# Kernel tuning notes

Measured on AMD Instinct MI355X. Metric: run time of the kernel, lower is better.

## Reference

```python
import math
import jax, jax.numpy as jnp
import numpy as np

D_MODEL = 1024
NUM_HEADS = 16
HEAD_DIM = D_MODEL // NUM_HEADS
CAUSAL = True


def setup_inputs() -> dict:
    key = jax.random.key(0)
    ks = jax.random.split(key, 9)
    B, S = 2, 2048
    s = 1.0 / math.sqrt(D_MODEL)
    x = jax.random.normal(ks[0], (B, S, D_MODEL), dtype=jnp.float32)
    Wq = jax.random.normal(ks[1], (D_MODEL, D_MODEL), dtype=jnp.float32) * s
    bq = jax.random.normal(ks[2], (D_MODEL,), dtype=jnp.float32) * 0.01
    Wk = jax.random.normal(ks[3], (D_MODEL, D_MODEL), dtype=jnp.float32) * s
    bk = jax.random.normal(ks[4], (D_MODEL,), dtype=jnp.float32) * 0.01
    Wv = jax.random.normal(ks[5], (D_MODEL, D_MODEL), dtype=jnp.float32) * s
    bv = jax.random.normal(ks[6], (D_MODEL,), dtype=jnp.float32) * 0.01
    Wo = jax.random.normal(ks[7], (D_MODEL, D_MODEL), dtype=jnp.float32) * s
    bo = jax.random.normal(ks[8], (D_MODEL,), dtype=jnp.float32) * 0.01
    return {"x": x, "Wq": Wq, "bq": bq, "Wk": Wk, "bk": bk,
            "Wv": Wv, "bv": bv, "Wo": Wo, "bo": bo}


def reference(x, Wq, bq, Wk, bk, Wv, bv, Wo, bo):
    B, S, _ = x.shape
    # projections (torch Linear: x @ W.T + b; here W already stored as [in,out])
    q = x @ Wq + bq
    k = x @ Wk + bk
    v = x @ Wv + bv
    # split heads -> [B, H, S, hd]
    def split(t):
        return t.reshape(B, S, NUM_HEADS, HEAD_DIM).transpose(0, 2, 1, 3)
    q, k, v = split(q), split(k), split(v)
    scores = jnp.einsum('bhqd,bhkd->bhqk', q, k) / math.sqrt(HEAD_DIM)
    if CAUSAL:
        causal = jnp.tril(jnp.ones((S, S), dtype=bool))  # True = keep
        scores = jnp.where(causal, scores, -jnp.inf)
    attn = jax.nn.softmax(scores, axis=-1)
    out = jnp.einsum('bhqk,bhkd->bhqd', attn, v)
    out = out.transpose(0, 2, 1, 3).reshape(B, S, D_MODEL)
    return out @ Wo + bo
```

## Files before the change

### kernel.cpp

```cpp
#include <hip/hip_runtime.h>
#include <hip/hip_bf16.h>

typedef __bf16 bf16_t;
typedef __bf16 v8bf __attribute__((ext_vector_type(8)));
typedef float  v4f  __attribute__((ext_vector_type(4)));

#define MFMA16(a, b, c) __builtin_amdgcn_mfma_f32_16x16x32_bf16((a), (b), (c), 0, 0, 0)

#define GLDS16(g, l) __builtin_amdgcn_global_load_lds(                         \
    (const __attribute__((address_space(1))) void*)(g),                        \
    (__attribute__((address_space(3))) void*)(l), 16, 0, 0)

#define VMEMCNT(n) asm volatile("s_waitcnt vmcnt(" #n ")" ::: "memory")
#define SBAR()     __builtin_amdgcn_s_barrier()
#define SFENCE()   __builtin_amdgcn_sched_barrier(0)

#define B_SZ   2
#define SEQ    2048
#define DM     1024
#define NH     16
#define HD     64
#define M_TOT  4096

#define QSCALE 0.18033688011112043f

__global__ __launch_bounds__(256)
void conv_x_kernel(const float* __restrict__ src, bf16_t* __restrict__ dst)
{
    int i = (blockIdx.x * 256 + threadIdx.x) * 8;
    float4 a = *reinterpret_cast<const float4*>(src + i);
    float4 b = *reinterpret_cast<const float4*>(src + i + 4);
    union { bf16_t h[8]; int4 v; } u;
    u.h[0] = (bf16_t)a.x; u.h[1] = (bf16_t)a.y; u.h[2] = (bf16_t)a.z; u.h[3] = (bf16_t)a.w;
    u.h[4] = (bf16_t)b.x; u.h[5] = (bf16_t)b.y; u.h[6] = (bf16_t)b.z; u.h[7] = (bf16_t)b.w;
    *reinterpret_cast<int4*>(dst + i) = u.v;
}

__global__ __launch_bounds__(256)
void conv_wt_kernel(const float* __restrict__ Wq, const float* __restrict__ Wk,
                    const float* __restrict__ Wv, const float* __restrict__ Wo,
                    bf16_t* __restrict__ WqkvT, bf16_t* __restrict__ WoT)
{
    __shared__ float t[32][33];
    const int z = blockIdx.z;
    const float* src = (z == 0) ? Wq : (z == 1) ? Wk : (z == 2) ? Wv : Wo;
    bf16_t* dst = (z < 3) ? (WqkvT + (size_t)z * 1048576) : WoT;
    const int tx = threadIdx.x & 31, ty = threadIdx.x >> 5;
    const int c0 = blockIdx.x * 32, r0 = blockIdx.y * 32;
#pragma unroll
    for (int i = 0; i < 4; ++i)
        t[ty + i * 8][tx] = src[(size_t)(r0 + ty + i * 8) * DM + c0 + tx];
    __syncthreads();
#pragma unroll
    for (int i = 0; i < 4; ++i)
        dst[(size_t)(c0 + ty + i * 8) * DM + r0 + tx] = (bf16_t)t[tx][ty + i * 8];
}

__global__ __launch_bounds__(256)
void gemm_qkv_kernel(const bf16_t* __restrict__ A, const bf16_t* __restrict__ BT,
                     const float* __restrict__ b0, const float* __restrict__ b1,
                     const float* __restrict__ b2,
                     bf16_t* __restrict__ oQ, bf16_t* __restrict__ oK,
                     bf16_t* __restrict__ oV)
{
    __shared__ __align__(16) bf16_t As[2 * 128 * 64];
    __shared__ __align__(16) bf16_t Bs[2 * 192 * 64];

    const int tid  = threadIdx.x;
    const int lane = tid & 63;
    const int wave = tid >> 6;
    const int wm   = (wave >> 1) * 64;
    const int wn   = (wave & 1) * 96;
    const int quad = lane >> 4;
    const int l15  = lane & 15;
    const int l7   = l15 & 7;

    const int n0 = blockIdx.x * 192;
    const int m0 = blockIdx.y * 128;

    const bf16_t *ap[4], *bp[6];
#pragma unroll
    for (int i = 0; i < 4; ++i) {
        int cidx = (wave * 4 + i) * 64 + lane;
        int r = cidx >> 3;
        int c = (cidx & 7) ^ (r & 7);
        ap[i] = A + (size_t)(m0 + r) * DM + c * 8;
    }
#pragma unroll
    for (int i = 0; i < 6; ++i) {
        int cidx = (wave * 6 + i) * 64 + lane;
        int r = cidx >> 3;
        int c = (cidx & 7) ^ (r & 7);
        bp[i] = BT + (size_t)(n0 + r) * DM + c * 8;
    }

    const v4f vzero = {0.f, 0.f, 0.f, 0.f};
    v4f acc[4][6];
#pragma unroll
    for (int mt = 0; mt < 4; ++mt)
#pragma unroll
        for (int nt = 0; nt < 6; ++nt) acc[mt][nt] = vzero;

#pragma unroll
    for (int i = 0; i < 4; ++i) { GLDS16(ap[i], As + (wave * 4 + i) * 512); ap[i] += 64; }
#pragma unroll
    for (int i = 0; i < 6; ++i) { GLDS16(bp[i], Bs + (wave * 6 + i) * 512); bp[i] += 64; }
#pragma unroll
    for (int i = 0; i < 4; ++i) { GLDS16(ap[i], As + 8192 + (wave * 4 + i) * 512); ap[i] += 64; }
#pragma unroll
    for (int i = 0; i < 6; ++i) { GLDS16(bp[i], Bs + 12288 + (wave * 6 + i) * 512); bp[i] += 64; }

    for (int it = 0; it < 16; ++it) {
        const int cur = it & 1;
        if (it < 15) { VMEMCNT(10); } else { VMEMCNT(0); }
        SBAR(); SFENCE();
#pragma unroll
        for (int ks = 0; ks < 2; ++ks) {
            v8bf af[4], bfq[6];
#pragma unroll
            for (int mt = 0; mt < 4; ++mt)
                af[mt] = *reinterpret_cast<const v8bf*>(
                    &As[cur * 8192 + (wm + mt * 16 + l15) * 64 + ((ks * 4 + quad) ^ l7) * 8]);
#pragma unroll
            for (int nt = 0; nt < 6; ++nt)
                bfq[nt] = *reinterpret_cast<const v8bf*>(
                    &Bs[cur * 12288 + (wn + nt * 16 + l15) * 64 + ((ks * 4 + quad) ^ l7) * 8]);
#pragma unroll
            for (int mt = 0; mt < 4; ++mt)
#pragma unroll
                for (int nt = 0; nt < 6; ++nt)
                    acc[mt][nt] = MFMA16(bfq[nt], af[mt], acc[mt][nt]);
        }
        SFENCE(); SBAR();
        if (it < 14) {
#pragma unroll
            for (int i = 0; i < 4; ++i) {
                GLDS16(ap[i], As + cur * 8192 + (wave * 4 + i) * 512);
                ap[i] += 64;
            }
#pragma unroll
            for (int i = 0; i < 6; ++i) {
                GLDS16(bp[i], Bs + cur * 12288 + (wave * 6 + i) * 512);
                bp[i] += 64;
            }
        }
    }

#pragma unroll
    for (int nt = 0; nt < 6; ++nt) {
        const int cf0 = n0 + wn + nt * 16;
        const int mat = cf0 >> 10;
        const int cw  = cf0 & 1023;
        if (mat != 2) {
            bf16_t* dst = (mat == 0) ? oQ : oK;
            const float scale = (mat == 0) ? QSCALE : 1.0f;
            const float* bias = (mat == 0) ? b0 : b1;
            const int h = cw >> 6;
            const int dbase = (cw & 63) + quad * 4;
            float4 bv = *reinterpret_cast<const float4*>(bias + cw + quad * 4);
#pragma unroll
            for (int mt = 0; mt < 4; ++mt) {
                int srow = m0 + wm + mt * 16 + l15;
                int b = srow >> 11, s = srow & 2047;
                union { bf16_t hh[4]; int2 v; } u;
                u.hh[0] = (bf16_t)((acc[mt][nt][0] + bv.x) * scale);
                u.hh[1] = (bf16_t)((acc[mt][nt][1] + bv.y) * scale);
                u.hh[2] = (bf16_t)((acc[mt][nt][2] + bv.z) * scale);
                u.hh[3] = (bf16_t)((acc[mt][nt][3] + bv.w) * scale);
                *reinterpret_cast<int2*>(
                    dst + ((size_t)(b * NH + h) * SEQ + s) * HD + dbase) = u.v;
            }
        } else {
#pragma unroll
            for (int r = 0; r < 4; ++r) {
                int cwe = cw + quad * 4 + r;
                float bvv = b2[cwe];
                int h = cwe >> 6, d = cwe & 63;
#pragma unroll
                for (int mt = 0; mt < 4; ++mt) {
                    int srow = m0 + wm + mt * 16 + l15;
                    int b = srow >> 11, s = srow & 2047;
                    oV[((size_t)(b * NH + h) * HD + d) * SEQ + s] =
                        (bf16_t)(acc[mt][nt][r] + bvv);
                }
            }
        }
    }
}

__global__ __launch_bounds__(256)
void gemm_o_kernel(const bf16_t* __restrict__ A, const bf16_t* __restrict__ BT,
                   const float* __restrict__ bias, float* __restrict__ out)
{
    __shared__ __align__(16) bf16_t As[2 * 128 * 64];
    __shared__ __align__(16) bf16_t Bs[2 * 64 * 64];

    const int tid  = threadIdx.x;
    const int lane = tid & 63;
    const int wave = tid >> 6;
    const int wm   = (wave >> 1) * 64;
    const int wn   = (wave & 1) * 32;
    const int quad = lane >> 4;
    const int l15  = lane & 15;
    const int l7   = l15 & 7;

    const int n0 = blockIdx.x * 64;
    const int m0 = blockIdx.y * 128;

    const bf16_t *ap[4], *bp[2];
#pragma unroll
    for (int i = 0; i < 4; ++i) {
        int cidx = (wave * 4 + i) * 64 + lane;
        int r = cidx >> 3;
        int c = (cidx & 7) ^ (r & 7);
        ap[i] = A + (size_t)(m0 + r) * DM + c * 8;
    }
#pragma unroll
    for (int i = 0; i < 2; ++i) {
        int cidx = (wave * 2 + i) * 64 + lane;
        int r = cidx >> 3;
        int c = (cidx & 7) ^ (r & 7);
        bp[i] = BT + (size_t)(n0 + r) * DM + c * 8;
    }

    const v4f vzero = {0.f, 0.f, 0.f, 0.f};
    v4f acc[4][2];
#pragma unroll
    for (int mt = 0; mt < 4; ++mt)
#pragma unroll
        for (int nt = 0; nt < 2; ++nt) acc[mt][nt] = vzero;

#pragma unroll
    for (int i = 0; i < 4; ++i) { GLDS16(ap[i], As + (wave * 4 + i) * 512); ap[i] += 64; }
#pragma unroll
    for (int i = 0; i < 2; ++i) { GLDS16(bp[i], Bs + (wave * 2 + i) * 512); bp[i] += 64; }
#pragma unroll
    for (int i = 0; i < 4; ++i) { GLDS16(ap[i], As + 8192 + (wave * 4 + i) * 512); ap[i] += 64; }
#pragma unroll
    for (int i = 0; i < 2; ++i) { GLDS16(bp[i], Bs + 4096 + (wave * 2 + i) * 512); bp[i] += 64; }

    for (int it = 0; it < 16; ++it) {
        const int cur = it & 1;
        if (it < 15) { VMEMCNT(6); } else { VMEMCNT(0); }
        SBAR(); SFENCE();
#pragma unroll
        for (int ks = 0; ks < 2; ++ks) {
            v8bf af[4], bfq[2];
#pragma unroll
            for (int mt = 0; mt < 4; ++mt)
                af[mt] = *reinterpret_cast<const v8bf*>(
                    &As[cur * 8192 + (wm + mt * 16 + l15) * 64 + ((ks * 4 + quad) ^ l7) * 8]);
#pragma unroll
            for (int nt = 0; nt < 2; ++nt)
                bfq[nt] = *reinterpret_cast<const v8bf*>(
                    &Bs[cur * 4096 + (wn + nt * 16 + l15) * 64 + ((ks * 4 + quad) ^ l7) * 8]);
#pragma unroll
            for (int mt = 0; mt < 4; ++mt)
#pragma unroll
                for (int nt = 0; nt < 2; ++nt)
                    acc[mt][nt] = MFMA16(af[mt], bfq[nt], acc[mt][nt]);
        }
        SFENCE(); SBAR();
        if (it < 14) {
#pragma unroll
            for (int i = 0; i < 4; ++i) {
                GLDS16(ap[i], As + cur * 8192 + (wave * 4 + i) * 512);
                ap[i] += 64;
            }
#pragma unroll
            for (int i = 0; i < 2; ++i) {
                GLDS16(bp[i], Bs + cur * 4096 + (wave * 2 + i) * 512);
                bp[i] += 64;
            }
        }
    }

#pragma unroll
    for (int mt = 0; mt < 4; ++mt) {
#pragma unroll
        for (int nt = 0; nt < 2; ++nt) {
            int col = n0 + wn + nt * 16 + l15;
            float bv = bias[col];
#pragma unroll
            for (int r = 0; r < 4; ++r) {
                int row = m0 + wm + mt * 16 + quad * 4 + r;
                out[(size_t)row * DM + col] = acc[mt][nt][r] + bv;
            }
        }
    }
}

__global__ __launch_bounds__(256)
void attn_kernel(const bf16_t* __restrict__ Q, const bf16_t* __restrict__ K,
                 const bf16_t* __restrict__ Vt, bf16_t* __restrict__ O)
{
    __shared__ __align__(16) bf16_t Ks[4][64 * 64];
    __shared__ __align__(16) bf16_t Vs[4][64 * 64];
    float* Ored = reinterpret_cast<float*>(&Ks[0][0]);
    float* lred = reinterpret_cast<float*>(&Vs[0][0]);

    const int tid  = threadIdx.x;
    const int lane = tid & 63;
    const int w    = tid >> 6;
    const int quad = lane >> 4;
    const int l15  = lane & 15;
    const int l7   = lane & 7;

    const int bid = blockIdx.x;
    const int xcd = bid & 7;
    const int j   = bid >> 3;
    const int bh  = (xcd << 2) | (j >> 4);
    const int p   = j & 15;
    const size_t base = (size_t)bh * SEQ * HD;
    const bf16_t* Qg = Q  + base;
    const bf16_t* Kg = K  + base;
    const bf16_t* Vg = Vt + base;

    const int rr0 = tid >> 3;
    const int cc0 = (tid & 7) ^ (rr0 & 7);
    const int bO = bh >> 4, hO = bh & 15;
    const v4f vzero = {0.f, 0.f, 0.f, 0.f};

    for (int phase = 0; phase < 2; ++phase) {
        const int t  = phase ? (31 - p) : p;
        const int q0 = t * 64;
        const int ns = (t + 2) >> 1;
        const bool tEven = ((t & 1) == 0);

        v8bf qf[4][2];
#pragma unroll
        for (int g = 0; g < 4; ++g) {
            const bf16_t* qrow = Qg + (size_t)(q0 + g * 16 + l15) * HD;
            qf[g][0] = *reinterpret_cast<const v8bf*>(qrow + quad * 8);
            qf[g][1] = *reinterpret_cast<const v8bf*>(qrow + 32 + quad * 8);
        }

        const bf16_t* kp0 = Kg + (size_t)rr0 * HD + cc0 * 8;
        const bf16_t* kp1 = kp0 + 32 * HD;
        const bf16_t* vp0 = Vg + (size_t)rr0 * SEQ + cc0 * 8;
        const bf16_t* vp1 = vp0 + (size_t)32 * SEQ;

        v4f acc_p[4][4];
#pragma unroll
        for (int dt = 0; dt < 4; ++dt)
#pragma unroll
            for (int g = 0; g < 4; ++g) acc_p[dt][g] = vzero;
        float lp[4] = {0.f, 0.f, 0.f, 0.f};

        VMEMCNT(0);
        SBAR();

#pragma unroll
        for (int s = 0; s < 2; ++s) {
            GLDS16(kp0, &Ks[s][w * 512]);  GLDS16(kp1, &Ks[s][2048 + w * 512]);
            GLDS16(vp0, &Vs[s][w * 512]);  GLDS16(vp1, &Vs[s][2048 + w * 512]);
            kp0 += 64 * HD;  kp1 += 64 * HD;  vp0 += 64;  vp1 += 64;
        }
        if (ns > 1) {
#pragma unroll
            for (int s = 2; s < 4; ++s) {
                GLDS16(kp0, &Ks[s][w * 512]);  GLDS16(kp1, &Ks[s][2048 + w * 512]);
                GLDS16(vp0, &Vs[s][w * 512]);  GLDS16(vp1, &Vs[s][2048 + w * 512]);
                kp0 += 64 * HD;  kp1 += 64 * HD;  vp0 += 64;  vp1 += 64;
            }
        }

        for (int si = 0; si < ns; ++si) {
            const int sA = (si & 1) * 2, sB = sA + 1;
            if (si + 1 < ns) { VMEMCNT(8); } else { VMEMCNT(0); }
            SBAR(); SFENCE();

            const bool last  = (si == ns - 1);
            const bool diagA = last && tEven;
            const bool diagB = last && !tEven;

            v4f stA[4], stB[4];
#pragma unroll
            for (int g = 0; g < 4; ++g) { stA[g] = vzero; stB[g] = vzero; }
#pragma unroll
            for (int ks = 0; ks < 2; ++ks) {
                const int koff = (16 * w + l15) * 64 + ((ks * 4 + quad) ^ l7) * 8;
                v8bf kfA = *reinterpret_cast<const v8bf*>(&Ks[sA][koff]);
                v8bf kfB = *reinterpret_cast<const v8bf*>(&Ks[sB][koff]);
#pragma unroll
                for (int g = 0; g < 4; ++g) {
                    stA[g] = MFMA16(kfA, qf[g][ks], stA[g]);
                    stB[g] = MFMA16(kfB, qf[g][ks], stB[g]);
                }
            }

            v8bf pa[4];
#pragma unroll
            for (int g = 0; g < 4; ++g) {
                union { bf16_t h[8]; v8bf v; } up;
                if (diagA && g < w) {
                    up.h[0] = (bf16_t)0.f; up.h[1] = (bf16_t)0.f;
                    up.h[2] = (bf16_t)0.f; up.h[3] = (bf16_t)0.f;
                } else if (diagA && g == w) {
#pragma unroll
                    for (int r = 0; r < 4; ++r) {
                        float pv = (quad * 4 + r > l15)
                                     ? 0.f : __builtin_amdgcn_exp2f(stA[g][r]);
                        lp[g] += pv;
                        up.h[r] = (bf16_t)pv;
                    }
                } else {
#pragma unroll
                    for (int r = 0; r < 4; ++r) {
                        float pv = __builtin_amdgcn_exp2f(stA[g][r]);
                        lp[g] += pv;
                        up.h[r] = (bf16_t)pv;
                    }
                }
                if (diagA || (diagB && g < w)) {
                    up.h[4] = (bf16_t)0.f; up.h[5] = (bf16_t)0.f;
                    up.h[6] = (bf16_t)0.f; up.h[7] = (bf16_t)0.f;
                } else if (diagB && g == w) {
#pragma unroll
                    for (int r = 0; r < 4; ++r) {
                        float pv = (quad * 4 + r > l15)
                                     ? 0.f : __builtin_amdgcn_exp2f(stB[g][r]);
                        lp[g] += pv;
                        up.h[4 + r] = (bf16_t)pv;
                    }
                } else {
#pragma unroll
                    for (int r = 0; r < 4; ++r) {
                        float pv = __builtin_amdgcn_exp2f(stB[g][r]);
                        lp[g] += pv;
                        up.h[4 + r] = (bf16_t)pv;
                    }
                }
                pa[g] = up.v;
            }

#pragma unroll
            for (int dt = 0; dt < 4; ++dt) {
                const int rowd = dt * 16 + l15;
                const int voff = rowd * 64 +
                    (((2 * w + (quad >> 1)) ^ l7) * 8 + (quad & 1) * 4);
                uint2 va = *reinterpret_cast<const uint2*>(&Vs[sA][voff]);
                uint2 vb = *reinterpret_cast<const uint2*>(&Vs[sB][voff]);
                union { unsigned u[4]; v8bf v; } uv;
                uv.u[0] = va.x; uv.u[1] = va.y; uv.u[2] = vb.x; uv.u[3] = vb.y;
#pragma unroll
                for (int g = 0; g < 4; ++g)
                    acc_p[dt][g] = MFMA16(uv.v, pa[g], acc_p[dt][g]);
            }

            SFENCE(); SBAR();
            if (si + 2 < ns) {
                GLDS16(kp0, &Ks[sA][w * 512]);  GLDS16(kp1, &Ks[sA][2048 + w * 512]);
                GLDS16(vp0, &Vs[sA][w * 512]);  GLDS16(vp1, &Vs[sA][2048 + w * 512]);
                kp0 += 64 * HD;  kp1 += 64 * HD;  vp0 += 64;  vp1 += 64;
                GLDS16(kp0, &Ks[sB][w * 512]);  GLDS16(kp1, &Ks[sB][2048 + w * 512]);
                GLDS16(vp0, &Vs[sB][w * 512]);  GLDS16(vp1, &Vs[sB][2048 + w * 512]);
                kp0 += 64 * HD;  kp1 += 64 * HD;  vp0 += 64;  vp1 += 64;
            }
        }

#pragma unroll
        for (int g = 0; g < 4; ++g) {
            lp[g] += __shfl_xor(lp[g], 16);
            lp[g] += __shfl_xor(lp[g], 32);
        }
        if (quad == 0) {
#pragma unroll
            for (int g = 0; g < 4; ++g)
                lred[w * 64 + g * 16 + l15] = lp[g];
        }

        const int qq = tid >> 2;
        const int db = (tid & 3) * 4;
        float linv = 0.f;
#pragma unroll
        for (int dt = 0; dt < 4; ++dt) {
#pragma unroll
            for (int g = 0; g < 4; ++g)
#pragma unroll
                for (int r = 0; r < 4; ++r)
                    Ored[w * 1040 + (quad * 4 + r) * 65 + g * 16 + l15] =
                        acc_p[dt][g][r];
            SBAR();
            if (dt == 0)
                linv = 1.f / (lred[qq] + lred[64 + qq] +
                              lred[128 + qq] + lred[192 + qq]);
            union { bf16_t h[4]; int2 v; } u;
#pragma unroll
            for (int e = 0; e < 4; ++e) {
                float s = Ored[(db + e) * 65 + qq]
                        + Ored[1040 + (db + e) * 65 + qq]
                        + Ored[2080 + (db + e) * 65 + qq]
                        + Ored[3120 + (db + e) * 65 + qq];
                u.h[e] = (bf16_t)(s * linv);
            }
            *reinterpret_cast<int2*>(
                &O[((size_t)bO * SEQ + q0 + qq) * DM + hO * 64 + dt * 16 + db]) = u.v;
            SBAR();
        }
    }
}

extern "C" void kernel_launch(void* const* d_in, const int* in_sizes, int n_in,
                              void* d_out, int out_size, void* d_ws, size_t ws_size,
                              hipStream_t stream) {
    const float* x  = (const float*)d_in[0];
    const float* Wq = (const float*)d_in[1];
    const float* bq = (const float*)d_in[2];
    const float* Wk = (const float*)d_in[3];
    const float* bk = (const float*)d_in[4];
    const float* Wv = (const float*)d_in[5];
    const float* bv = (const float*)d_in[6];
    const float* Wo = (const float*)d_in[7];
    const float* bo = (const float*)d_in[8];

    bf16_t* ws = (bf16_t*)d_ws;
    bf16_t* xb     = ws;
    bf16_t* WqkvT  = ws + 4194304;
    bf16_t* WoT    = ws + 7340032;
    bf16_t* Qb     = ws + 8388608;
    bf16_t* Kb     = ws + 12582912;
    bf16_t* Vb     = ws + 16777216;
    bf16_t* Ob     = ws;

    conv_x_kernel<<<2048, 256, 0, stream>>>(x, xb);
    conv_wt_kernel<<<dim3(32, 32, 4), 256, 0, stream>>>(Wq, Wk, Wv, Wo, WqkvT, WoT);
    gemm_qkv_kernel<<<dim3(16, 32), 256, 0, stream>>>(xb, WqkvT, bq, bk, bv, Qb, Kb, Vb);
    attn_kernel<<<512, 256, 0, stream>>>(Qb, Kb, Vb, Ob);
    gemm_o_kernel<<<dim3(16, 32), 256, 0, stream>>>(Ob, WoT, bo, (float*)d_out);
}
```

Baseline: 173.8 us.

## Shrink GEMM tiles and drop LDS double buffering to raise block count

The QKV GEMM moves from 128x192 tiles to 128x128 tiles, with one Q, K or V matrix per block column, giving a 24x32 grid. The O-projection GEMM moves to 64x64 tiles with 128 threads, giving a 16x64 grid. Both kernels drop the double-buffered LDS pipeline and its explicit vmcnt waits for a single buffer guarded by __syncthreads. The aim is more blocks and occupancy on the many-CU device, at the cost of exposed load latency and less operand reuse per tile.

```diff
diff --git a/kernel.cpp b/kernel.cpp
--- a/kernel.cpp
+++ b/kernel.cpp
@@ -63,101 +63,86 @@
                      bf16_t* __restrict__ oQ, bf16_t* __restrict__ oK,
                      bf16_t* __restrict__ oV)
 {
-    __shared__ __align__(16) bf16_t As[2 * 128 * 64];
-    __shared__ __align__(16) bf16_t Bs[2 * 192 * 64];
+    __shared__ __align__(16) bf16_t As[128 * 64];
+    __shared__ __align__(16) bf16_t Bs[128 * 64];
 
     const int tid  = threadIdx.x;
     const int lane = tid & 63;
     const int wave = tid >> 6;
     const int wm   = (wave >> 1) * 64;
-    const int wn   = (wave & 1) * 96;
+    const int wn   = (wave & 1) * 64;
     const int quad = lane >> 4;
     const int l15  = lane & 15;
     const int l7   = l15 & 7;
 
-    const int n0 = blockIdx.x * 192;
-    const int m0 = blockIdx.y * 128;
-
-    const bf16_t *ap[4], *bp[6];
+    const int mat = blockIdx.x >> 3;
+    const int n0  = (blockIdx.x & 7) * 128;
+    const int m0  = blockIdx.y * 128;
+    const bf16_t* Bmat = BT + (size_t)mat * 1048576;
+
+    const bf16_t *ap[4], *bp[4];
 #pragma unroll
     for (int i = 0; i < 4; ++i) {
         int cidx = (wave * 4 + i) * 64 + lane;
         int r = cidx >> 3;
         int c = (cidx & 7) ^ (r & 7);
-        ap[i] = A + (size_t)(m0 + r) * DM + c * 8;
-    }
-#pragma unroll
-    for (int i = 0; i < 6; ++i) {
-        int cidx = (wave * 6 + i) * 64 + lane;
-        int r = cidx >> 3;
-        int c = (cidx & 7) ^ (r & 7);
-        bp[i] = BT + (size_t)(n0 + r) * DM + c * 8;
+        ap[i] = A    + (size_t)(m0 + r) * DM + c * 8;
+        bp[i] = Bmat + (size_t)(n0 + r) * DM + c * 8;
     }
 
     const v4f vzero = {0.f, 0.f, 0.f, 0.f};
-    v4f acc[4][6];
+    v4f acc[4][4];
 #pragma unroll
     for (int mt = 0; mt < 4; ++mt)
 #pragma unroll
-        for (int nt = 0; nt < 6; ++nt) acc[mt][nt] = vzero;
-
-#pragma unroll
-    for (int i = 0; i < 4; ++i) { GLDS16(ap[i], As + (wave * 4 + i) * 512); ap[i] += 64; }
-#pragma unroll
-    for (int i = 0; i < 6; ++i) { GLDS16(bp[i], Bs + (wave * 6 + i) * 512); bp[i] += 64; }
-#pragma unroll
-    for (int i = 0; i < 4; ++i) { GLDS16(ap[i], As + 8192 + (wave * 4 + i) * 512); ap[i] += 64; }
-#pragma unroll
-    for (int i = 0; i < 6; ++i) { GLDS16(bp[i], Bs + 12288 + (wave * 6 + i) * 512); bp[i] += 64; }
+        for (int nt = 0; nt < 4; ++nt) acc[mt][nt] = vzero;
+
+#pragma unroll
+    for (int i = 0; i < 4; ++i) {
+        GLDS16(ap[i], As + (wave * 4 + i) * 512);
+        GLDS16(bp[i], Bs + (wave * 4 + i) * 512);
+        ap[i] += 64; bp[i] += 64;
+    }
 
     for (int it = 0; it < 16; ++it) {
-        const int cur = it & 1;
-        if (it < 15) { VMEMCNT(10); } else { VMEMCNT(0); }
-        SBAR(); SFENCE();
+        __syncthreads();
 #pragma unroll
         for (int ks = 0; ks < 2; ++ks) {
-            v8bf af[4], bfq[6];
+            v8bf af[4], bfq[4];
 #pragma unroll
             for (int mt = 0; mt < 4; ++mt)
                 af[mt] = *reinterpret_cast<const v8bf*>(
-                    &As[cur * 8192 + (wm + mt * 16 + l15) * 64 + ((ks * 4 + quad) ^ l7) * 8]);
-#pragma unroll
-            for (int nt = 0; nt < 6; ++nt)
+                    &As[(wm + mt * 16 + l15) * 64 + ((ks * 4 + quad) ^ l7) * 8]);
+#pragma unroll
+            for (int nt = 0; nt < 4; ++nt)
                 bfq[nt] = *reinterpret_cast<const v8bf*>(
-                    &Bs[cur * 12288 + (wn + nt * 16 + l15) * 64 + ((ks * 4 + quad) ^ l7) * 8]);
+                    &Bs[(wn + nt * 16 + l15) * 64 + ((ks * 4 + quad) ^ l7) * 8]);
 #pragma unroll
             for (int mt = 0; mt < 4; ++mt)
 #pragma unroll
-                for (int nt = 0; nt < 6; ++nt)
+                for (int nt = 0; nt < 4; ++nt)
                     acc[mt][nt] = MFMA16(bfq[nt], af[mt], acc[mt][nt]);
         }
-        SFENCE(); SBAR();
-        if (it < 14) {
+        __syncthreads();
+        if (it < 15) {
 #pragma unroll
             for (int i = 0; i < 4; ++i) {
-                GLDS16(ap[i], As + cur * 8192 + (wave * 4 + i) * 512);
-                ap[i] += 64;
-            }
-#pragma unroll
-            for (int i = 0; i < 6; ++i) {
-                GLDS16(bp[i], Bs + cur * 12288 + (wave * 6 + i) * 512);
-                bp[i] += 64;
-            }
-        }
-    }
-
-#pragma unroll
-    for (int nt = 0; nt < 6; ++nt) {
-        const int cf0 = n0 + wn + nt * 16;
-        const int mat = cf0 >> 10;
-        const int cw  = cf0 & 1023;
-        if (mat != 2) {
-            bf16_t* dst = (mat == 0) ? oQ : oK;
-            const float scale = (mat == 0) ? QSCALE : 1.0f;
-            const float* bias = (mat == 0) ? b0 : b1;
-            const int h = cw >> 6;
-            const int dbase = (cw & 63) + quad * 4;
-            float4 bv = *reinterpret_cast<const float4*>(bias + cw + quad * 4);
+                GLDS16(ap[i], As + (wave * 4 + i) * 512);
+                GLDS16(bp[i], Bs + (wave * 4 + i) * 512);
+                ap[i] += 64; bp[i] += 64;
+            }
+        }
+    }
+
+    const float* bias = (mat == 0) ? b0 : (mat == 1) ? b1 : b2;
+    if (mat != 2) {
+        bf16_t* dst = (mat == 0) ? oQ : oK;
+        const float scale = (mat == 0) ? QSCALE : 1.0f;
+        const int h = (n0 + wn) >> 6;
+#pragma unroll
+        for (int nt = 0; nt < 4; ++nt) {
+            const int dbase = nt * 16 + quad * 4;
+            float4 bv = *reinterpret_cast<const float4*>(bias + n0 + wn + dbase);
 #pragma unroll
             for (int mt = 0; mt < 4; ++mt) {
                 int srow = m0 + wm + mt * 16 + l15;
@@ -170,116 +155,104 @@
                 *reinterpret_cast<int2*>(
                     dst + ((size_t)(b * NH + h) * SEQ + s) * HD + dbase) = u.v;
             }
-        } else {
+        }
+    } else {
+#pragma unroll
+        for (int nt = 0; nt < 4; ++nt) {
 #pragma unroll
             for (int r = 0; r < 4; ++r) {
-                int cwe = cw + quad * 4 + r;
-                float bvv = b2[cwe];
-                int h = cwe >> 6, d = cwe & 63;
+                int coln = n0 + wn + nt * 16 + quad * 4 + r;
+                float bv = bias[coln];
+                int h = coln >> 6, d = coln & 63;
 #pragma unroll
                 for (int mt = 0; mt < 4; ++mt) {
                     int srow = m0 + wm + mt * 16 + l15;
                     int b = srow >> 11, s = srow & 2047;
                     oV[((size_t)(b * NH + h) * HD + d) * SEQ + s] =
-                        (bf16_t)(acc[mt][nt][r] + bvv);
+                        (bf16_t)(acc[mt][nt][r] + bv);
                 }
             }
         }
     }
 }
 
-__global__ __launch_bounds__(256)
+__global__ __launch_bounds__(128)
 void gemm_o_kernel(const bf16_t* __restrict__ A, const bf16_t* __restrict__ BT,
                    const float* __restrict__ bias, float* __restrict__ out)
 {
-    __shared__ __align__(16) bf16_t As[2 * 128 * 64];
-    __shared__ __align__(16) bf16_t Bs[2 * 64 * 64];
+    __shared__ __align__(16) bf16_t As[64 * 64];
+    __shared__ __align__(16) bf16_t Bs[64 * 64];
 
     const int tid  = threadIdx.x;
     const int lane = tid & 63;
     const int wave = tid >> 6;
-    const int wm   = (wave >> 1) * 64;
-    const int wn   = (wave & 1) * 32;
+    const int wm   = wave * 32;
     const int quad = lane >> 4;
     const int l15  = lane & 15;
     const int l7   = l15 & 7;
 
     const int n0 = blockIdx.x * 64;
-    const int m0 = blockIdx.y * 128;
-
-    const bf16_t *ap[4], *bp[2];
+    const int m0 = blockIdx.y * 64;
+
+    const bf16_t *ap[4], *bp[4];
 #pragma unroll
     for (int i = 0; i < 4; ++i) {
-        int cidx = (wave * 4 + i) * 64 + lane;
+        int cidx = wave * 64 + i * 128 + lane;
         int r = cidx >> 3;
         int c = (cidx & 7) ^ (r & 7);
-        ap[i] = A + (size_t)(m0 + r) * DM + c * 8;
-    }
-#pragma unroll
-    for (int i = 0; i < 2; ++i) {
-        int cidx = (wave * 2 + i) * 64 + lane;
-        int r = cidx >> 3;
-        int c = (cidx & 7) ^ (r & 7);
+        ap[i] = A  + (size_t)(m0 + r) * DM + c * 8;
         bp[i] = BT + (size_t)(n0 + r) * DM + c * 8;
     }
 
     const v4f vzero = {0.f, 0.f, 0.f, 0.f};
-    v4f acc[4][2];
-#pragma unroll
-    for (int mt = 0; mt < 4; ++mt)
-#pragma unroll
-        for (int nt = 0; nt < 2; ++nt) acc[mt][nt] = vzero;
-
-#pragma unroll
-    for (int i = 0; i < 4; ++i) { GLDS16(ap[i], As + (wave * 4 + i) * 512); ap[i] += 64; }
-#pragma unroll
-    for (int i = 0; i < 2; ++i) { GLDS16(bp[i], Bs + (wave * 2 + i) * 512); bp[i] += 64; }
-#pragma unroll
-    for (int i = 0; i < 4; ++i) { GLDS16(ap[i], As + 8192 + (wave * 4 + i) * 512); ap[i] += 64; }
-#pragma unroll
-    for (int i = 0; i < 2; ++i) { GLDS16(bp[i], Bs + 4096 + (wave * 2 + i) * 512); bp[i] += 64; }
+    v4f acc[2][4];
+#pragma unroll
+    for (int mt = 0; mt < 2; ++mt)
+#pragma unroll
+        for (int nt = 0; nt < 4; ++nt) acc[mt][nt] = vzero;
+
+#pragma unroll
+    for (int i = 0; i < 4; ++i) {
+        GLDS16(ap[i], As + wave * 512 + i * 1024);
+        GLDS16(bp[i], Bs + wave * 512 + i * 1024);
+        ap[i] += 64; bp[i] += 64;
+    }
 
     for (int it = 0; it < 16; ++it) {
-        const int cur = it & 1;
-        if (it < 15) { VMEMCNT(6); } else { VMEMCNT(0); }
-        SBAR(); SFENCE();
+        __syncthreads();
 #pragma unroll
         for (int ks = 0; ks < 2; ++ks) {
-            v8bf af[4], bfq[2];
-#pragma unroll
-            for (int mt = 0; mt < 4; ++mt)
+            v8bf af[2], bfq[4];
+#pragma unroll
+            for (int mt = 0; mt < 2; ++mt)
                 af[mt] = *reinterpret_cast<const v8bf*>(
-                    &As[cur * 8192 + (wm + mt * 16 + l15) * 64 + ((ks * 4 + quad) ^ l7) * 8]);
-#pragma unroll
-            for (int nt = 0; nt < 2; ++nt)
+                    &As[(wm + mt * 16 + l15) * 64 + ((ks * 4 + quad) ^ l7) * 8]);
+#pragma unroll
+            for (int nt = 0; nt < 4; ++nt)
                 bfq[nt] = *reinterpret_cast<const v8bf*>(
-                    &Bs[cur * 4096 + (wn + nt * 16 + l15) * 64 + ((ks * 4 + quad) ^ l7) * 8]);
-#pragma unroll
-            for (int mt = 0; mt < 4; ++mt)
-#pragma unroll
-                for (int nt = 0; nt < 2; ++nt)
+                    &Bs[(nt * 16 + l15) * 64 + ((ks * 4 + quad) ^ l7) * 8]);
+#pragma unroll
+            for (int mt = 0; mt < 2; ++mt)
+#pragma unroll
+                for (int nt = 0; nt < 4; ++nt)
                     acc[mt][nt] = MFMA16(af[mt], bfq[nt], acc[mt][nt]);
         }
-        SFENCE(); SBAR();
-        if (it < 14) {
+        __syncthreads();
+        if (it < 15) {
 #pragma unroll
             for (int i = 0; i < 4; ++i) {
-                GLDS16(ap[i], As + cur * 8192 + (wave * 4 + i) * 512);
-                ap[i] += 64;
-            }
-#pragma unroll
-            for (int i = 0; i < 2; ++i) {
-                GLDS16(bp[i], Bs + cur * 4096 + (wave * 2 + i) * 512);
-                bp[i] += 64;
-            }
-        }
-    }
-
-#pragma unroll
-    for (int mt = 0; mt < 4; ++mt) {
-#pragma unroll
-        for (int nt = 0; nt < 2; ++nt) {
-            int col = n0 + wn + nt * 16 + l15;
+                GLDS16(ap[i], As + wave * 512 + i * 1024);
+                GLDS16(bp[i], Bs + wave * 512 + i * 1024);
+                ap[i] += 64; bp[i] += 64;
+            }
+        }
+    }
+
+#pragma unroll
+    for (int mt = 0; mt < 2; ++mt) {
+#pragma unroll
+        for (int nt = 0; nt < 4; ++nt) {
+            int col = n0 + nt * 16 + l15;
             float bv = bias[col];
 #pragma unroll
             for (int r = 0; r < 4; ++r) {
@@ -525,7 +498,7 @@
 
     conv_x_kernel<<<2048, 256, 0, stream>>>(x, xb);
     conv_wt_kernel<<<dim3(32, 32, 4), 256, 0, stream>>>(Wq, Wk, Wv, Wo, WqkvT, WoT);
-    gemm_qkv_kernel<<<dim3(16, 32), 256, 0, stream>>>(xb, WqkvT, bq, bk, bv, Qb, Kb, Vb);
+    gemm_qkv_kernel<<<dim3(24, 32), 256, 0, stream>>>(xb, WqkvT, bq, bk, bv, Qb, Kb, Vb);
     attn_kernel<<<512, 256, 0, stream>>>(Qb, Kb, Vb, Ob);
-    gemm_o_kernel<<<dim3(16, 32), 256, 0, stream>>>(Ob, WoT, bo, (float*)d_out);
+    gemm_o_kernel<<<dim3(16, 64), 128, 0, stream>>>(Ob, WoT, bo, (float*)d_out);
 }
```

Measured after the change: 180.3 us. 3.7% more time.

## Shrink output-projection GEMM tile to 64x64 with two waves and single buffer

Applied to the files above, without the earlier changes.

The output-projection GEMM tile shrinks from 128x64 to 64x64 and runs on 128 threads (two waves, each computing 32x64), which doubles the grid to 1024 blocks. The LDS double buffer and its explicit vmcnt waits are replaced by one buffer guarded by __syncthreads. The goal is better fill across the GPU's compute units, with less LDS and register use per block. In exchange, loads no longer overlap compute within a block, each tile reuses less data, and more global traffic goes to re-reading A and B.

```diff
diff --git a/kernel.cpp b/kernel.cpp
--- a/kernel.cpp
+++ b/kernel.cpp
@@ -188,98 +188,83 @@
     }
 }
 
-__global__ __launch_bounds__(256)
+__global__ __launch_bounds__(128)
 void gemm_o_kernel(const bf16_t* __restrict__ A, const bf16_t* __restrict__ BT,
                    const float* __restrict__ bias, float* __restrict__ out)
 {
-    __shared__ __align__(16) bf16_t As[2 * 128 * 64];
-    __shared__ __align__(16) bf16_t Bs[2 * 64 * 64];
+    __shared__ __align__(16) bf16_t As[64 * 64];
+    __shared__ __align__(16) bf16_t Bs[64 * 64];
 
     const int tid  = threadIdx.x;
     const int lane = tid & 63;
     const int wave = tid >> 6;
-    const int wm   = (wave >> 1) * 64;
-    const int wn   = (wave & 1) * 32;
+    const int wm   = wave * 32;
     const int quad = lane >> 4;
     const int l15  = lane & 15;
     const int l7   = l15 & 7;
 
     const int n0 = blockIdx.x * 64;
-    const int m0 = blockIdx.y * 128;
-
-    const bf16_t *ap[4], *bp[2];
+    const int m0 = blockIdx.y * 64;
+
+    const bf16_t *ap[4], *bp[4];
 #pragma unroll
     for (int i = 0; i < 4; ++i) {
-        int cidx = (wave * 4 + i) * 64 + lane;
+        int cidx = wave * 64 + i * 128 + lane;
         int r = cidx >> 3;
         int c = (cidx & 7) ^ (r & 7);
-        ap[i] = A + (size_t)(m0 + r) * DM + c * 8;
-    }
-#pragma unroll
-    for (int i = 0; i < 2; ++i) {
-        int cidx = (wave * 2 + i) * 64 + lane;
-        int r = cidx >> 3;
-        int c = (cidx & 7) ^ (r & 7);
+        ap[i] = A  + (size_t)(m0 + r) * DM + c * 8;
         bp[i] = BT + (size_t)(n0 + r) * DM + c * 8;
     }
 
     const v4f vzero = {0.f, 0.f, 0.f, 0.f};
-    v4f acc[4][2];
-#pragma unroll
-    for (int mt = 0; mt < 4; ++mt)
-#pragma unroll
-        for (int nt = 0; nt < 2; ++nt) acc[mt][nt] = vzero;
-
-#pragma unroll
-    for (int i = 0; i < 4; ++i) { GLDS16(ap[i], As + (wave * 4 + i) * 512); ap[i] += 64; }
-#pragma unroll
-    for (int i = 0; i < 2; ++i) { GLDS16(bp[i], Bs + (wave * 2 + i) * 512); bp[i] += 64; }
-#pragma unroll
-    for (int i = 0; i < 4; ++i) { GLDS16(ap[i], As + 8192 + (wave * 4 + i) * 512); ap[i] += 64; }
-#pragma unroll
-    for (int i = 0; i < 2; ++i) { GLDS16(bp[i], Bs + 4096 + (wave * 2 + i) * 512); bp[i] += 64; }
+    v4f acc[2][4];
+#pragma unroll
+    for (int mt = 0; mt < 2; ++mt)
+#pragma unroll
+        for (int nt = 0; nt < 4; ++nt) acc[mt][nt] = vzero;
+
+#pragma unroll
+    for (int i = 0; i < 4; ++i) {
+        GLDS16(ap[i], As + wave * 512 + i * 1024);
+        GLDS16(bp[i], Bs + wave * 512 + i * 1024);
+        ap[i] += 64; bp[i] += 64;
+    }
 
     for (int it = 0; it < 16; ++it) {
-        const int cur = it & 1;
-        if (it < 15) { VMEMCNT(6); } else { VMEMCNT(0); }
-        SBAR(); SFENCE();
+        __syncthreads();
 #pragma unroll
         for (int ks = 0; ks < 2; ++ks) {
-            v8bf af[4], bfq[2];
-#pragma unroll
-            for (int mt = 0; mt < 4; ++mt)
+            v8bf af[2], bfq[4];
+#pragma unroll
+            for (int mt = 0; mt < 2; ++mt)
                 af[mt] = *reinterpret_cast<const v8bf*>(
-                    &As[cur * 8192 + (wm + mt * 16 + l15) * 64 + ((ks * 4 + quad) ^ l7) * 8]);
-#pragma unroll
-            for (int nt = 0; nt < 2; ++nt)
+                    &As[(wm + mt * 16 + l15) * 64 + ((ks * 4 + quad) ^ l7) * 8]);
+#pragma unroll
+            for (int nt = 0; nt < 4; ++nt)
                 bfq[nt] = *reinterpret_cast<const v8bf*>(
-                    &Bs[cur * 4096 + (wn + nt * 16 + l15) * 64 + ((ks * 4 + quad) ^ l7) * 8]);
-#pragma unroll
-            for (int mt = 0; mt < 4; ++mt)
-#pragma unroll
-                for (int nt = 0; nt < 2; ++nt)
+                    &Bs[(nt * 16 + l15) * 64 + ((ks * 4 + quad) ^ l7) * 8]);
+#pragma unroll
+            for (int mt = 0; mt < 2; ++mt)
+#pragma unroll
+                for (int nt = 0; nt < 4; ++nt)
                     acc[mt][nt] = MFMA16(af[mt], bfq[nt], acc[mt][nt]);
         }
-        SFENCE(); SBAR();
-        if (it < 14) {
+        __syncthreads();
+        if (it < 15) {
 #pragma unroll
             for (int i = 0; i < 4; ++i) {
-                GLDS16(ap[i], As + cur * 8192 + (wave * 4 + i) * 512);
-                ap[i] += 64;
-            }
-#pragma unroll
-            for (int i = 0; i < 2; ++i) {
-                GLDS16(bp[i], Bs + cur * 4096 + (wave * 2 + i) * 512);
-                bp[i] += 64;
-            }
-        }
-    }
-
-#pragma unroll
-    for (int mt = 0; mt < 4; ++mt) {
-#pragma unroll
-        for (int nt = 0; nt < 2; ++nt) {
-            int col = n0 + wn + nt * 16 + l15;
+                GLDS16(ap[i], As + wave * 512 + i * 1024);
+                GLDS16(bp[i], Bs + wave * 512 + i * 1024);
+                ap[i] += 64; bp[i] += 64;
+            }
+        }
+    }
+
+#pragma unroll
+    for (int mt = 0; mt < 2; ++mt) {
+#pragma unroll
+        for (int nt = 0; nt < 4; ++nt) {
+            int col = n0 + nt * 16 + l15;
             float bv = bias[col];
 #pragma unroll
             for (int r = 0; r < 4; ++r) {
@@ -527,5 +512,5 @@
     conv_wt_kernel<<<dim3(32, 32, 4), 256, 0, stream>>>(Wq, Wk, Wv, Wo, WqkvT, WoT);
     gemm_qkv_kernel<<<dim3(16, 32), 256, 0, stream>>>(xb, WqkvT, bq, bk, bv, Qb, Kb, Vb);
     attn_kernel<<<512, 256, 0, stream>>>(Qb, Kb, Vb, Ob);
-    gemm_o_kernel<<<dim3(16, 32), 256, 0, stream>>>(Ob, WoT, bo, (float*)d_out);
+    gemm_o_kernel<<<dim3(16, 64), 128, 0, stream>>>(Ob, WoT, bo, (float*)d_out);
 }
```

After: 175.5 us. No clear change (+1.0%).
